# Optimization experiments

Hardware: AMD Instinct MI355X
Metric: run time of the kernel (lower is better)

The kernel has to match this reference:

```python
import jax, jax.numpy as jnp
import numpy as np

DEPTH, DIM, HEADS, DIM_HEAD, MLP = 6, 768, 12, 64, 3072
INNER = HEADS * DIM_HEAD  # 768
EPS = 1e-5


def _layernorm(x, w, b):
    m = jnp.mean(x, axis=-1, keepdims=True)
    v = jnp.mean((x - m) ** 2, axis=-1, keepdims=True)
    return (x - m) * jax.lax.rsqrt(v + EPS) * w + b


def setup_inputs() -> dict:
    key = jax.random.key(0)
    ks = jax.random.split(key, 12)
    s = 0.02
    return {
        "x": jax.random.normal(ks[0], (4, 1024, DIM), dtype=jnp.float32),
        "ln1_w": jnp.ones((DEPTH, DIM), jnp.float32),
        "ln1_b": jnp.zeros((DEPTH, DIM), jnp.float32),
        "w_qkv": jax.random.normal(ks[1], (DEPTH, DIM, 3 * INNER), jnp.float32) * s,
        "w_o": jax.random.normal(ks[2], (DEPTH, INNER, DIM), jnp.float32) * s,
        "b_o": jnp.zeros((DEPTH, DIM), jnp.float32),
        "ln2_w": jnp.ones((DEPTH, DIM), jnp.float32),
        "ln2_b": jnp.zeros((DEPTH, DIM), jnp.float32),
        "w1": jax.random.normal(ks[3], (DEPTH, DIM, MLP), jnp.float32) * s,
        "b1": jnp.zeros((DEPTH, MLP), jnp.float32),
        "w2": jax.random.normal(ks[4], (DEPTH, MLP, DIM), jnp.float32) * s,
        "b2": jnp.zeros((DEPTH, DIM), jnp.float32),
    }


def _forward(x, ln1_w, ln1_b, w_qkv, w_o, b_o, ln2_w, ln2_b, w1, b1, w2, b2):
    scale = DIM_HEAD ** -0.5
    b, n, _ = x.shape

    def block(x, p):
        l1w, l1b, wqkv, wo, bo, l2w, l2b, W1, B1, W2, B2 = p
        # --- attention (pre-norm); dropout/droppath are identity in eval ---
        h = _layernorm(x, l1w, l1b)
        qkv = h @ wqkv                                   # [b, n, 3*inner]
        q, k, v = jnp.split(qkv, 3, axis=-1)
        q = q.reshape(b, n, HEADS, DIM_HEAD).transpose(0, 2, 1, 3)
        k = k.reshape(b, n, HEADS, DIM_HEAD).transpose(0, 2, 1, 3)
        v = v.reshape(b, n, HEADS, DIM_HEAD).transpose(0, 2, 1, 3)
        dots = jnp.einsum('bhid,bhjd->bhij', q, k) * scale   # [b, h, n, n]
        attn = jax.nn.softmax(dots, axis=-1)
        out = jnp.einsum('bhij,bhjd->bhid', attn, v)
        out = out.transpose(0, 2, 1, 3).reshape(b, n, INNER)
        x = x + out @ wo + bo
        # --- feed-forward (pre-norm), exact GELU like torch default ---
        h = _layernorm(x, l2w, l2b)
        x = x + jax.nn.gelu(h @ W1 + B1, approximate=False) @ W2 + B2
        return x, None

    x, _ = jax.lax.scan(block, x, (ln1_w, ln1_b, w_qkv, w_o, b_o,
                                   ln2_w, ln2_b, w1, b1, w2, b2))
    return x


def reference(x, ln1_w, ln1_b, w_qkv, w_o, b_o, ln2_w, ln2_b, w1, b1, w2, b2):
    return _forward(x, ln1_w, ln1_b, w_qkv, w_o, b_o, ln2_w, ln2_b, w1, b1, w2, b2)
```

## Files before the change

### kernel.cpp

```cpp
#include <hip/hip_runtime.h>
#include <cmath>
#include <cstdint>

typedef __bf16 bf16_t;
typedef __bf16 bf16x8 __attribute__((ext_vector_type(8)));
typedef __bf16 bf16x4 __attribute__((ext_vector_type(4)));
typedef float  f32x4  __attribute__((ext_vector_type(4)));

#define DEPTH 6
#define DIM   768
#define HEADS 12
#define DH    64
#define MLPD  3072
#define SEQ   1024
#define BATCH 4
#define MTOT  (BATCH*SEQ)
#define QKVN  2304

static __device__ __forceinline__ bf16x8 ld8(const bf16_t* p) {
    return *(const bf16x8*)p;
}

typedef const __attribute__((address_space(1))) unsigned int gas_u32;
typedef __attribute__((address_space(3))) unsigned int las_u32;
static __device__ __forceinline__ void gload16(const bf16_t* g, bf16_t* l) {
    __builtin_amdgcn_global_load_lds((gas_u32*)g, (las_u32*)l, 16, 0, 0);
}

__global__ __launch_bounds__(256) void tcvt_kernel(const float* __restrict__ in,
                                                   bf16_t* __restrict__ out,
                                                   int K, int N) {
    __shared__ float ts[32][33];
    int n0 = blockIdx.x * 32, k0 = blockIdx.y * 32;
    size_t base = (size_t)blockIdx.z * K * N;
    int tx = threadIdx.x & 31, ty = threadIdx.x >> 5;
    #pragma unroll
    for (int r = 0; r < 32; r += 8)
        ts[ty + r][tx] = in[base + (size_t)(k0 + ty + r) * N + n0 + tx];
    __syncthreads();
    #pragma unroll
    for (int r = 0; r < 32; r += 8)
        out[base + (size_t)(n0 + ty + r) * K + k0 + tx] = (bf16_t)ts[tx][ty + r];
}

__global__ __launch_bounds__(256) void lnr_kernel(const float* __restrict__ xin,
                                                  float* __restrict__ xout,
                                                  const float* __restrict__ P,
                                                  int nslices,
                                                  const float* __restrict__ bias,
                                                  const float* __restrict__ w,
                                                  const float* __restrict__ b,
                                                  bf16_t* __restrict__ h,
                                                  int writeLN) {
    int row = blockIdx.x, t = threadIdx.x;
    size_t ro = (size_t)row * DIM;
    float v[3];
    #pragma unroll
    for (int e = 0; e < 3; e++) {
        int c = t + e * 256;
        float xv = xin[ro + c];
        if (nslices) {
            xv += bias[c];
            for (int s = 0; s < nslices; s++)
                xv += P[(size_t)s * MTOT * DIM + ro + c];
        }
        v[e] = xv;
    }
    if (nslices) {
        #pragma unroll
        for (int e = 0; e < 3; e++) xout[ro + t + e * 256] = v[e];
    }
    float s = v[0] + v[1] + v[2];
    float q = v[0] * v[0] + v[1] * v[1] + v[2] * v[2];
    #pragma unroll
    for (int off = 32; off > 0; off >>= 1) {
        s += __shfl_down(s, off);
        q += __shfl_down(q, off);
    }
    __shared__ float ss[4], sq[4], stat[2];
    if ((t & 63) == 0) { ss[t >> 6] = s; sq[t >> 6] = q; }
    __syncthreads();
    if (t == 0) {
        float S = ss[0] + ss[1] + ss[2] + ss[3];
        float Q = sq[0] + sq[1] + sq[2] + sq[3];
        float mean = S * (1.0f / DIM);
        float var  = Q * (1.0f / DIM) - mean * mean;
        stat[0] = mean;
        stat[1] = rsqrtf(var + 1e-5f);
    }
    __syncthreads();
    if (writeLN) {
        float mean = stat[0], rstd = stat[1];
        #pragma unroll
        for (int e = 0; e < 3; e++) {
            int c = t + e * 256;
            h[ro + c] = (bf16_t)((v[e] - mean) * rstd * w[c] + b[c]);
        }
    }
}

template <int EPI>
__global__ __launch_bounds__(256) void gemm_kernel(const bf16_t* __restrict__ A,
                                                   const bf16_t* __restrict__ Bt,
                                                   const float* __restrict__ bias,
                                                   bf16_t* __restrict__ Cb,
                                                   float* __restrict__ Cf,
                                                   bf16_t* __restrict__ Vt,
                                                   int N, int K, int klen) {
    __shared__ __align__(16) bf16_t As[2][128 * 32];
    __shared__ __align__(16) bf16_t Bs[2][128 * 32];
    int t = threadIdx.x;
    int m0 = blockIdx.y * 128, n0 = blockIdx.x * 128;
    int kz = blockIdx.z;
    int kbeg = kz * klen, kend = kbeg + klen;
    int lane = t & 63, l16 = lane & 15, quad = lane >> 4;
    int wv = t >> 6, wm = wv >> 1, wn = wv & 1;
    f32x4 acc[4][4] = {};

    int srow = wv * 16 + (lane >> 2);
    int skc  = (lane & 3) * 8;
    const bf16_t* ga = A  + (size_t)(m0 + srow) * K + skc;
    const bf16_t* gb = Bt + (size_t)(n0 + srow) * K + skc;
    size_t rh = (size_t)64 * K;

    for (int k0 = kbeg; k0 < kend; k0 += 64) {
        __syncthreads();
        #pragma unroll
        for (int p = 0; p < 2; p++) {
            gload16(ga + k0 + p * 32,      &As[p][(wv * 16) * 32]);
            gload16(ga + rh + k0 + p * 32, &As[p][(64 + wv * 16) * 32]);
            gload16(gb + k0 + p * 32,      &Bs[p][(wv * 16) * 32]);
            gload16(gb + rh + k0 + p * 32, &Bs[p][(64 + wv * 16) * 32]);
        }
        __syncthreads();
        #pragma unroll
        for (int p = 0; p < 2; p++) {
            bf16x8 af[4], bfr[4];
            #pragma unroll
            for (int i = 0; i < 4; i++)
                af[i] = ld8(&As[p][(wm * 64 + i * 16 + l16) * 32 + quad * 8]);
            #pragma unroll
            for (int j = 0; j < 4; j++)
                bfr[j] = ld8(&Bs[p][(wn * 64 + j * 16 + l16) * 32 + quad * 8]);
            #pragma unroll
            for (int i = 0; i < 4; i++)
                #pragma unroll
                for (int j = 0; j < 4; j++)
                    acc[i][j] = __builtin_amdgcn_mfma_f32_16x16x32_bf16(af[i], bfr[j], acc[i][j], 0, 0, 0);
        }
    }

    if constexpr (EPI == 0) {
        if (n0 >= 1536) {
            int b = m0 >> 10;
            #pragma unroll
            for (int i = 0; i < 4; i++) {
                int n = (m0 & 1023) + wm * 64 + i * 16 + quad * 4;
                #pragma unroll
                for (int j = 0; j < 4; j++) {
                    int hc = n0 + wn * 64 + j * 16 + l16 - 1536;
                    int hh = hc >> 6, d = hc & 63;
                    bf16x4 ov;
                    #pragma unroll
                    for (int r = 0; r < 4; r++) ov[r] = (bf16_t)acc[i][j][r];
                    *(bf16x4*)&Vt[(((size_t)b * HEADS + hh) * 64 + d) * SEQ + n] = ov;
                }
            }
            return;
        }
    }
    #pragma unroll
    for (int i = 0; i < 4; i++) {
        int grow = m0 + wm * 64 + i * 16 + quad * 4;
        #pragma unroll
        for (int j = 0; j < 4; j++) {
            int gcol = n0 + wn * 64 + j * 16 + l16;
            float bv = 0.0f;
            if constexpr (EPI == 1) bv = bias[gcol];
            #pragma unroll
            for (int r = 0; r < 4; r++) {
                size_t idx = (size_t)(grow + r) * N + gcol;
                float v = acc[i][j][r];
                if constexpr (EPI == 0) {
                    Cb[idx] = (bf16_t)v;
                } else if constexpr (EPI == 1) {
                    v += bv;
                    v = 0.5f * v * (1.0f + erff(v * 0.70710678118654752f));
                    Cb[idx] = (bf16_t)v;
                } else {
                    Cf[(size_t)kz * MTOT * N + idx] = v;
                }
            }
        }
    }
}

__global__ __launch_bounds__(256) void attn_kernel(const bf16_t* __restrict__ qkv,
                                                   const bf16_t* __restrict__ vt,
                                                   bf16_t* __restrict__ out) {
    int qt = blockIdx.x, h = blockIdx.y, b = blockIdx.z;
    int t = threadIdx.x;
    int wv = t >> 6, lane = t & 63, l16 = lane & 15, quad = lane >> 4;
    const float LOG2E = 1.44269504f;
    int qw0 = qt * 64 + wv * 16;

    __shared__ __align__(16) bf16_t Ks[2][64 * 32];
    __shared__ __align__(16) bf16_t Vs[64 * 64];
    __shared__ __align__(16) bf16_t Pa[4][16 * 72];
    bf16_t* P = Pa[wv];

    size_t bS = (size_t)b * SEQ;
    const bf16_t* qrow = qkv + (bS + qw0 + l16) * QKVN + h * 64;
    bf16x8 qf0 = ld8(qrow + quad * 8);
    bf16x8 qf1 = ld8(qrow + 32 + quad * 8);

    float m = -3e38f, l = 0.0f;
    f32x4 o[4] = {};

    const bf16_t* kbase = qkv + bS * QKVN + 768 + h * 64;
    const bf16_t* vbase = vt + ((size_t)(b * HEADS + h) * 64) * SEQ;

    for (int kb = 0; kb < SEQ; kb += 64) {
        __syncthreads();
        if (wv < 2) {
            #pragma unroll
            for (int j = 0; j < 4; j++) {
                int i = wv * 4 + j, p = i & 1, rg = i >> 1;
                gload16(kbase + (size_t)(kb + rg * 16 + (lane >> 2)) * QKVN
                              + p * 32 + (lane & 3) * 8,
                        &Ks[p][rg * 16 * 32]);
            }
        } else {
            #pragma unroll
            for (int j = 0; j < 4; j++) {
                int dg = (wv - 2) * 4 + j;
                gload16(vbase + (size_t)(dg * 8 + (lane >> 3)) * SEQ
                              + kb + (lane & 7) * 8,
                        &Vs[dg * 8 * 64]);
            }
        }
        __syncthreads();

        f32x4 s[4];
        #pragma unroll
        for (int tt = 0; tt < 4; tt++) {
            f32x4 z = {};
            z = __builtin_amdgcn_mfma_f32_16x16x32_bf16(
                    ld8(&Ks[0][(tt * 16 + l16) * 32 + quad * 8]), qf0, z, 0, 0, 0);
            z = __builtin_amdgcn_mfma_f32_16x16x32_bf16(
                    ld8(&Ks[1][(tt * 16 + l16) * 32 + quad * 8]), qf1, z, 0, 0, 0);
            s[tt] = z;
        }
        float mx = -3e38f;
        #pragma unroll
        for (int tt = 0; tt < 4; tt++)
            #pragma unroll
            for (int r = 0; r < 4; r++) {
                s[tt][r] *= 0.125f;
                mx = fmaxf(mx, s[tt][r]);
            }
        mx = fmaxf(mx, __shfl_xor(mx, 16));
        mx = fmaxf(mx, __shfl_xor(mx, 32));
        float mn = fmaxf(m, mx);
        float alpha = exp2f((m - mn) * LOG2E);
        m = mn;
        float nb = mn * LOG2E;
        float rs = 0.0f;
        #pragma unroll
        for (int tt = 0; tt < 4; tt++) {
            bf16x4 pkt;
            #pragma unroll
            for (int r = 0; r < 4; r++) {
                float p = exp2f(fmaf(s[tt][r], LOG2E, -nb));
                rs += p;
                pkt[r] = (bf16_t)p;
            }
            *(bf16x4*)&P[l16 * 72 + tt * 16 + quad * 4] = pkt;
        }
        l = l * alpha + rs;
        #pragma unroll
        for (int jt = 0; jt < 4; jt++) o[jt] *= alpha;
        asm volatile("s_waitcnt lgkmcnt(0)" ::: "memory");
        bf16x8 pf0 = ld8(&P[l16 * 72 + quad * 8]);
        bf16x8 pf1 = ld8(&P[l16 * 72 + 32 + quad * 8]);
        #pragma unroll
        for (int jt = 0; jt < 4; jt++) {
            const bf16_t* vp = &Vs[(jt * 16 + l16) * 64];
            o[jt] = __builtin_amdgcn_mfma_f32_16x16x32_bf16(ld8(vp + quad * 8), pf0, o[jt], 0, 0, 0);
            o[jt] = __builtin_amdgcn_mfma_f32_16x16x32_bf16(ld8(vp + 32 + quad * 8), pf1, o[jt], 0, 0, 0);
        }
    }

    l += __shfl_xor(l, 16);
    l += __shfl_xor(l, 32);
    float inv = 1.0f / l;
    bf16_t* orow = out + (bS + qw0 + l16) * DIM + h * 64;
    #pragma unroll
    for (int jt = 0; jt < 4; jt++) {
        bf16x4 ov;
        #pragma unroll
        for (int r = 0; r < 4; r++) ov[r] = (bf16_t)(o[jt][r] * inv);
        *(bf16x4*)&orow[jt * 16 + quad * 4] = ov;
    }
}

extern "C" void kernel_launch(void* const* d_in, const int* in_sizes, int n_in,
                              void* d_out, int out_size, void* d_ws, size_t ws_size,
                              hipStream_t stream) {
    const float* x     = (const float*)d_in[0];
    const float* ln1_w = (const float*)d_in[1];
    const float* ln1_b = (const float*)d_in[2];
    const float* w_qkv = (const float*)d_in[3];
    const float* w_o   = (const float*)d_in[4];
    const float* b_o   = (const float*)d_in[5];
    const float* ln2_w = (const float*)d_in[6];
    const float* ln2_b = (const float*)d_in[7];
    const float* w1    = (const float*)d_in[8];
    const float* b1    = (const float*)d_in[9];
    const float* w2    = (const float*)d_in[10];
    const float* b2    = (const float*)d_in[11];
    float* out = (float*)d_out;

    char* ws = (char*)d_ws;
    size_t off = 0;
    auto alloc = [&](size_t bytes) -> char* {
        char* p = ws + off;
        off += (bytes + 255) & ~(size_t)255;
        return p;
    };
    bf16_t* wqkv_t = (bf16_t*)alloc((size_t)DEPTH * DIM * QKVN * 2);
    bf16_t* wo_t   = (bf16_t*)alloc((size_t)DEPTH * DIM * DIM * 2);
    bf16_t* w1_t   = (bf16_t*)alloc((size_t)DEPTH * DIM * MLPD * 2);
    bf16_t* w2_t   = (bf16_t*)alloc((size_t)DEPTH * MLPD * DIM * 2);
    bf16_t* hbuf   = (bf16_t*)alloc((size_t)MTOT * DIM * 2);
    bf16_t* qkvb   = (bf16_t*)alloc((size_t)MTOT * QKVN * 2);
    bf16_t* vtb    = (bf16_t*)alloc((size_t)BATCH * HEADS * 64 * SEQ * 2);
    bf16_t* aob    = (bf16_t*)alloc((size_t)MTOT * DIM * 2);
    bf16_t* midb   = (bf16_t*)alloc((size_t)MTOT * MLPD * 2);
    float*  Pm     = (float*)alloc((size_t)4 * MTOT * DIM * 4);
    float*  Pp     = (float*)qkvb;
    if (off > ws_size) return;

    tcvt_kernel<<<dim3(QKVN / 32, DIM / 32, DEPTH), 256, 0, stream>>>(w_qkv, wqkv_t, DIM, QKVN);
    tcvt_kernel<<<dim3(DIM / 32,  DIM / 32, DEPTH), 256, 0, stream>>>(w_o,   wo_t,   DIM, DIM);
    tcvt_kernel<<<dim3(MLPD / 32, DIM / 32, DEPTH), 256, 0, stream>>>(w1,    w1_t,   DIM, MLPD);
    tcvt_kernel<<<dim3(DIM / 32, MLPD / 32, DEPTH), 256, 0, stream>>>(w2,    w2_t,   MLPD, DIM);

    hipMemcpyAsync(out, x, (size_t)MTOT * DIM * 4, hipMemcpyDeviceToDevice, stream);

    lnr_kernel<<<MTOT, 256, 0, stream>>>(out, out, nullptr, 0, nullptr,
                                         ln1_w, ln1_b, hbuf, 1);

    for (int L = 0; L < DEPTH; L++) {
        gemm_kernel<0><<<dim3(QKVN / 128, MTOT / 128, 1), 256, 0, stream>>>(
            hbuf, wqkv_t + (size_t)L * DIM * QKVN, nullptr, qkvb, nullptr, vtb,
            QKVN, DIM, DIM);
        attn_kernel<<<dim3(SEQ / 64, HEADS, BATCH), 256, 0, stream>>>(qkvb, vtb, aob);
        gemm_kernel<2><<<dim3(DIM / 128, MTOT / 128, 2), 256, 0, stream>>>(
            aob, wo_t + (size_t)L * DIM * DIM, nullptr, nullptr, Pp, nullptr,
            DIM, DIM, 384);
        lnr_kernel<<<MTOT, 256, 0, stream>>>(out, out, Pp, 2, b_o + L * DIM,
                                             ln2_w + L * DIM, ln2_b + L * DIM, hbuf, 1);
        gemm_kernel<1><<<dim3(MLPD / 128, MTOT / 128, 1), 256, 0, stream>>>(
            hbuf, w1_t + (size_t)L * DIM * MLPD, b1 + L * MLPD, midb, nullptr, nullptr,
            MLPD, DIM, DIM);
        gemm_kernel<2><<<dim3(DIM / 128, MTOT / 128, 4), 256, 0, stream>>>(
            midb, w2_t + (size_t)L * MLPD * DIM, nullptr, nullptr, Pm, nullptr,
            DIM, MLPD, 768);
        if (L < DEPTH - 1) {
            lnr_kernel<<<MTOT, 256, 0, stream>>>(out, out, Pm, 4, b2 + L * DIM,
                                                 ln1_w + (L + 1) * DIM,
                                                 ln1_b + (L + 1) * DIM, hbuf, 1);
        } else {
            lnr_kernel<<<MTOT, 256, 0, stream>>>(out, out, Pm, 4, b2 + L * DIM,
                                                 ln1_w, ln1_b, hbuf, 0);
        }
    }
}
```

Baseline: 1.346 ms.

## Double-buffer GEMM and attention loads with swizzled LDS, vectorize layernorm

The GEMM main loop moves from loading a 64-wide K chunk and then computing with two barriers, to a double-buffered 32-wide K pipeline with one barrier per iteration. Its LDS layout is XOR-swizzled to avoid bank conflicts. The attention kernel likewise double-buffers K and V tiles with a swizzled 64-wide layout, so the next tile's global loads overlap the current tile's MFMA work. The layernorm/residual kernel now uses 192 threads with float4 loads and bf16x4 stores. The cost is more LDS per block in attention and a smaller K step per barrier in the GEMM.

```diff
diff --git a/kernel.cpp b/kernel.cpp
--- a/kernel.cpp
+++ b/kernel.cpp
@@ -43,7 +43,7 @@
         out[base + (size_t)(n0 + ty + r) * K + k0 + tx] = (bf16_t)ts[tx][ty + r];
 }
 
-__global__ __launch_bounds__(256) void lnr_kernel(const float* __restrict__ xin,
+__global__ __launch_bounds__(192) void lnr_kernel(const float* __restrict__ xin,
                                                   float* __restrict__ xout,
                                                   const float* __restrict__ P,
                                                   int nslices,
@@ -53,36 +53,30 @@
                                                   bf16_t* __restrict__ h,
                                                   int writeLN) {
     int row = blockIdx.x, t = threadIdx.x;
-    size_t ro = (size_t)row * DIM;
-    float v[3];
-    #pragma unroll
-    for (int e = 0; e < 3; e++) {
-        int c = t + e * 256;
-        float xv = xin[ro + c];
-        if (nslices) {
-            xv += bias[c];
-            for (int s = 0; s < nslices; s++)
-                xv += P[(size_t)s * MTOT * DIM + ro + c];
-        }
-        v[e] = xv;
-    }
+    size_t r4 = (size_t)row * 192 + t;
+    float4 v = ((const float4*)xin)[r4];
     if (nslices) {
-        #pragma unroll
-        for (int e = 0; e < 3; e++) xout[ro + t + e * 256] = v[e];
-    }
-    float s = v[0] + v[1] + v[2];
-    float q = v[0] * v[0] + v[1] * v[1] + v[2] * v[2];
+        float4 bi = ((const float4*)bias)[t];
+        v.x += bi.x; v.y += bi.y; v.z += bi.z; v.w += bi.w;
+        for (int s = 0; s < nslices; s++) {
+            float4 pv = ((const float4*)P)[(size_t)s * MTOT * 192 + r4];
+            v.x += pv.x; v.y += pv.y; v.z += pv.z; v.w += pv.w;
+        }
+        ((float4*)xout)[r4] = v;
+    }
+    float s = v.x + v.y + v.z + v.w;
+    float q = v.x * v.x + v.y * v.y + v.z * v.z + v.w * v.w;
     #pragma unroll
     for (int off = 32; off > 0; off >>= 1) {
         s += __shfl_down(s, off);
         q += __shfl_down(q, off);
     }
-    __shared__ float ss[4], sq[4], stat[2];
+    __shared__ float ss[3], sq[3], stat[2];
     if ((t & 63) == 0) { ss[t >> 6] = s; sq[t >> 6] = q; }
     __syncthreads();
     if (t == 0) {
-        float S = ss[0] + ss[1] + ss[2] + ss[3];
-        float Q = sq[0] + sq[1] + sq[2] + sq[3];
+        float S = ss[0] + ss[1] + ss[2];
+        float Q = sq[0] + sq[1] + sq[2];
         float mean = S * (1.0f / DIM);
         float var  = Q * (1.0f / DIM) - mean * mean;
         stat[0] = mean;
@@ -91,11 +85,14 @@
     __syncthreads();
     if (writeLN) {
         float mean = stat[0], rstd = stat[1];
-        #pragma unroll
-        for (int e = 0; e < 3; e++) {
-            int c = t + e * 256;
-            h[ro + c] = (bf16_t)((v[e] - mean) * rstd * w[c] + b[c]);
-        }
+        float4 wv4 = ((const float4*)w)[t];
+        float4 bv4 = ((const float4*)b)[t];
+        bf16x4 o;
+        o[0] = (bf16_t)((v.x - mean) * rstd * wv4.x + bv4.x);
+        o[1] = (bf16_t)((v.y - mean) * rstd * wv4.y + bv4.y);
+        o[2] = (bf16_t)((v.z - mean) * rstd * wv4.z + bv4.z);
+        o[3] = (bf16_t)((v.w - mean) * rstd * wv4.w + bv4.w);
+        *(bf16x4*)&h[(size_t)row * DIM + t * 4] = o;
     }
 }
 
@@ -112,42 +109,51 @@
     int t = threadIdx.x;
     int m0 = blockIdx.y * 128, n0 = blockIdx.x * 128;
     int kz = blockIdx.z;
-    int kbeg = kz * klen, kend = kbeg + klen;
+    int kbeg = kz * klen;
     int lane = t & 63, l16 = lane & 15, quad = lane >> 4;
     int wv = t >> 6, wm = wv >> 1, wn = wv & 1;
     f32x4 acc[4][4] = {};
 
-    int srow = wv * 16 + (lane >> 2);
-    int skc  = (lane & 3) * 8;
-    const bf16_t* ga = A  + (size_t)(m0 + srow) * K + skc;
-    const bf16_t* gb = Bt + (size_t)(n0 + srow) * K + skc;
-    size_t rh = (size_t)64 * K;
-
-    for (int k0 = kbeg; k0 < kend; k0 += 64) {
+    int sr = lane >> 2;
+    int sc = ((lane & 3) ^ ((lane >> 3) & 3)) * 8;
+    const bf16_t* gA0 = A  + (size_t)(m0 + wv * 32 + sr) * K + sc;
+    const bf16_t* gA1 = gA0 + (size_t)16 * K;
+    const bf16_t* gB0 = Bt + (size_t)(n0 + wv * 32 + sr) * K + sc;
+    const bf16_t* gB1 = gB0 + (size_t)16 * K;
+    bf16_t* lA0 = &As[0][(wv * 32) * 32];
+    bf16_t* lA1 = &As[0][(wv * 32 + 16) * 32];
+    bf16_t* lB0 = &Bs[0][(wv * 32) * 32];
+    bf16_t* lB1 = &Bs[0][(wv * 32 + 16) * 32];
+    const int bufoff = 128 * 32;
+
+    auto stage = [&](int buf, int k0) {
+        gload16(gA0 + k0, lA0 + buf * bufoff);
+        gload16(gA1 + k0, lA1 + buf * bufoff);
+        gload16(gB0 + k0, lB0 + buf * bufoff);
+        gload16(gB1 + k0, lB1 + buf * bufoff);
+    };
+
+    int nIt = klen >> 5;
+    stage(0, kbeg);
+    int posA = (quad ^ ((l16 >> 1) & 3)) * 8;
+
+    for (int it = 0; it < nIt; it++) {
         __syncthreads();
-        #pragma unroll
-        for (int p = 0; p < 2; p++) {
-            gload16(ga + k0 + p * 32,      &As[p][(wv * 16) * 32]);
-            gload16(ga + rh + k0 + p * 32, &As[p][(64 + wv * 16) * 32]);
-            gload16(gb + k0 + p * 32,      &Bs[p][(wv * 16) * 32]);
-            gload16(gb + rh + k0 + p * 32, &Bs[p][(64 + wv * 16) * 32]);
-        }
-        __syncthreads();
-        #pragma unroll
-        for (int p = 0; p < 2; p++) {
-            bf16x8 af[4], bfr[4];
-            #pragma unroll
-            for (int i = 0; i < 4; i++)
-                af[i] = ld8(&As[p][(wm * 64 + i * 16 + l16) * 32 + quad * 8]);
+        if (it + 1 < nIt) stage((it + 1) & 1, kbeg + (it + 1) * 32);
+        const bf16_t* as = As[it & 1];
+        const bf16_t* bs = Bs[it & 1];
+        bf16x8 af[4], bfr[4];
+        #pragma unroll
+        for (int i = 0; i < 4; i++)
+            af[i] = ld8(&as[(wm * 64 + i * 16 + l16) * 32 + posA]);
+        #pragma unroll
+        for (int j = 0; j < 4; j++)
+            bfr[j] = ld8(&bs[(wn * 64 + j * 16 + l16) * 32 + posA]);
+        #pragma unroll
+        for (int i = 0; i < 4; i++)
             #pragma unroll
             for (int j = 0; j < 4; j++)
-                bfr[j] = ld8(&Bs[p][(wn * 64 + j * 16 + l16) * 32 + quad * 8]);
-            #pragma unroll
-            for (int i = 0; i < 4; i++)
-                #pragma unroll
-                for (int j = 0; j < 4; j++)
-                    acc[i][j] = __builtin_amdgcn_mfma_f32_16x16x32_bf16(af[i], bfr[j], acc[i][j], 0, 0, 0);
-        }
+                acc[i][j] = __builtin_amdgcn_mfma_f32_16x16x32_bf16(af[i], bfr[j], acc[i][j], 0, 0, 0);
     }
 
     if constexpr (EPI == 0) {
@@ -204,8 +210,8 @@
     const float LOG2E = 1.44269504f;
     int qw0 = qt * 64 + wv * 16;
 
-    __shared__ __align__(16) bf16_t Ks[2][64 * 32];
-    __shared__ __align__(16) bf16_t Vs[64 * 64];
+    __shared__ __align__(16) bf16_t Ks[2][64 * 64];
+    __shared__ __align__(16) bf16_t Vs[2][64 * 64];
     __shared__ __align__(16) bf16_t Pa[4][16 * 72];
     bf16_t* P = Pa[wv];
 
@@ -220,35 +226,38 @@
     const bf16_t* kbase = qkv + bS * QKVN + 768 + h * 64;
     const bf16_t* vbase = vt + ((size_t)(b * HEADS + h) * 64) * SEQ;
 
-    for (int kb = 0; kb < SEQ; kb += 64) {
+    int ar = lane >> 3;
+    int ac = ((lane & 7) ^ ar) * 8;
+    int i0 = wv * 2, i1 = wv * 2 + 1;
+    const bf16_t* gK0 = kbase + (size_t)(i0 * 8 + ar) * QKVN + ac;
+    const bf16_t* gK1 = kbase + (size_t)(i1 * 8 + ar) * QKVN + ac;
+    const bf16_t* gV0 = vbase + (size_t)(i0 * 8 + ar) * SEQ + ac;
+    const bf16_t* gV1 = vbase + (size_t)(i1 * 8 + ar) * SEQ + ac;
+
+    auto stage = [&](int buf, int kb) {
+        gload16(gK0 + (size_t)kb * QKVN, &Ks[buf][i0 * 8 * 64]);
+        gload16(gK1 + (size_t)kb * QKVN, &Ks[buf][i1 * 8 * 64]);
+        gload16(gV0 + kb, &Vs[buf][i0 * 8 * 64]);
+        gload16(gV1 + kb, &Vs[buf][i1 * 8 * 64]);
+    };
+
+    stage(0, 0);
+    int p0 = (quad ^ (l16 & 7)) * 8;
+    int p1 = ((quad + 4) ^ (l16 & 7)) * 8;
+
+    for (int it = 0; it < SEQ / 64; it++) {
         __syncthreads();
-        if (wv < 2) {
-            #pragma unroll
-            for (int j = 0; j < 4; j++) {
-                int i = wv * 4 + j, p = i & 1, rg = i >> 1;
-                gload16(kbase + (size_t)(kb + rg * 16 + (lane >> 2)) * QKVN
-                              + p * 32 + (lane & 3) * 8,
-                        &Ks[p][rg * 16 * 32]);
-            }
-        } else {
-            #pragma unroll
-            for (int j = 0; j < 4; j++) {
-                int dg = (wv - 2) * 4 + j;
-                gload16(vbase + (size_t)(dg * 8 + (lane >> 3)) * SEQ
-                              + kb + (lane & 7) * 8,
-                        &Vs[dg * 8 * 64]);
-            }
-        }
-        __syncthreads();
+        if (it + 1 < SEQ / 64) stage((it + 1) & 1, (it + 1) * 64);
+        const bf16_t* ks = Ks[it & 1];
+        const bf16_t* vs = Vs[it & 1];
 
         f32x4 s[4];
         #pragma unroll
         for (int tt = 0; tt < 4; tt++) {
+            const bf16_t* kr = &ks[(tt * 16 + l16) * 64];
             f32x4 z = {};
-            z = __builtin_amdgcn_mfma_f32_16x16x32_bf16(
-                    ld8(&Ks[0][(tt * 16 + l16) * 32 + quad * 8]), qf0, z, 0, 0, 0);
-            z = __builtin_amdgcn_mfma_f32_16x16x32_bf16(
-                    ld8(&Ks[1][(tt * 16 + l16) * 32 + quad * 8]), qf1, z, 0, 0, 0);
+            z = __builtin_amdgcn_mfma_f32_16x16x32_bf16(ld8(kr + p0), qf0, z, 0, 0, 0);
+            z = __builtin_amdgcn_mfma_f32_16x16x32_bf16(ld8(kr + p1), qf1, z, 0, 0, 0);
             s[tt] = z;
         }
         float mx = -3e38f;
@@ -285,9 +294,9 @@
         bf16x8 pf1 = ld8(&P[l16 * 72 + 32 + quad * 8]);
         #pragma unroll
         for (int jt = 0; jt < 4; jt++) {
-            const bf16_t* vp = &Vs[(jt * 16 + l16) * 64];
-            o[jt] = __builtin_amdgcn_mfma_f32_16x16x32_bf16(ld8(vp + quad * 8), pf0, o[jt], 0, 0, 0);
-            o[jt] = __builtin_amdgcn_mfma_f32_16x16x32_bf16(ld8(vp + 32 + quad * 8), pf1, o[jt], 0, 0, 0);
+            const bf16_t* vr = &vs[(jt * 16 + l16) * 64];
+            o[jt] = __builtin_amdgcn_mfma_f32_16x16x32_bf16(ld8(vr + p0), pf0, o[jt], 0, 0, 0);
+            o[jt] = __builtin_amdgcn_mfma_f32_16x16x32_bf16(ld8(vr + p1), pf1, o[jt], 0, 0, 0);
         }
     }
 
@@ -348,7 +357,7 @@
 
     hipMemcpyAsync(out, x, (size_t)MTOT * DIM * 4, hipMemcpyDeviceToDevice, stream);
 
-    lnr_kernel<<<MTOT, 256, 0, stream>>>(out, out, nullptr, 0, nullptr,
+    lnr_kernel<<<MTOT, 192, 0, stream>>>(out, out, nullptr, 0, nullptr,
                                          ln1_w, ln1_b, hbuf, 1);
 
     for (int L = 0; L < DEPTH; L++) {
@@ -359,7 +368,7 @@
         gemm_kernel<2><<<dim3(DIM / 128, MTOT / 128, 2), 256, 0, stream>>>(
             aob, wo_t + (size_t)L * DIM * DIM, nullptr, nullptr, Pp, nullptr,
             DIM, DIM, 384);
-        lnr_kernel<<<MTOT, 256, 0, stream>>>(out, out, Pp, 2, b_o + L * DIM,
+        lnr_kernel<<<MTOT, 192, 0, stream>>>(out, out, Pp, 2, b_o + L * DIM,
                                              ln2_w + L * DIM, ln2_b + L * DIM, hbuf, 1);
         gemm_kernel<1><<<dim3(MLPD / 128, MTOT / 128, 1), 256, 0, stream>>>(
             hbuf, w1_t + (size_t)L * DIM * MLPD, b1 + L * MLPD, midb, nullptr, nullptr,
@@ -368,11 +377,11 @@
             midb, w2_t + (size_t)L * MLPD * DIM, nullptr, nullptr, Pm, nullptr,
             DIM, MLPD, 768);
         if (L < DEPTH - 1) {
-            lnr_kernel<<<MTOT, 256, 0, stream>>>(out, out, Pm, 4, b2 + L * DIM,
+            lnr_kernel<<<MTOT, 192, 0, stream>>>(out, out, Pm, 4, b2 + L * DIM,
                                                  ln1_w + (L + 1) * DIM,
                                                  ln1_b + (L + 1) * DIM, hbuf, 1);
         } else {
-            lnr_kernel<<<MTOT, 256, 0, stream>>>(out, out, Pm, 4, b2 + L * DIM,
+            lnr_kernel<<<MTOT, 192, 0, stream>>>(out, out, Pm, 4, b2 + L * DIM,
                                                  ln1_w, ln1_b, hbuf, 0);
         }
     }
```

After: 1.287 ms. -4.3%, faster.
